# Kernel optimization log

Measured on AMD Instinct MI355X. Metric: run time of the kernel, lower is better.

Reference implementation:

```python
import jax, jax.numpy as jnp
import numpy as np
import math

D_MODEL = 1024
N_HEADS = 16
D_HEAD = D_MODEL // N_HEADS


def _pos_encoding(seq_len, d_model):
    # matches get_pos_encoding: paired frequencies (repeat_interleave(2)),
    # sin on even columns, cos on odd columns of the SAME angle matrix.
    position = jnp.arange(seq_len, dtype=jnp.float32)[:, None]          # [L,1]
    div = 1.0 / (10000.0 ** (jnp.arange(0, d_model, 2, dtype=jnp.float32) / d_model))
    div = jnp.repeat(div, 2)[None, :]                                    # [1,D]
    ang = position * div                                                 # [L,D]
    col = jnp.arange(d_model)
    return jnp.where(col[None, :] % 2 == 0, jnp.sin(ang), jnp.cos(ang))


def _rel_enc_shift(a):
    # a: [b, h, l, m] -> Transformer-XL relative shift
    b, h, l, m = a.shape
    a = jnp.concatenate([a, jnp.zeros((b, h, l, 1), a.dtype)], axis=-1)  # [b,h,l,m+1]
    a = a.reshape(b, h, l * (m + 1))
    a = a[:, :, l - 1: l - 1 + l * m]
    return a.reshape(b, h, l, m)


def setup_inputs() -> dict:
    key = jax.random.key(0)
    ks = jax.random.split(key, 10)
    B, S, D = 1, 2048, D_MODEL
    s = 1.0 / math.sqrt(D)
    inp = {
        "query": jax.random.normal(ks[0], (B, S, D), jnp.float32),
        "key": jax.random.normal(ks[1], (B, S, D), jnp.float32),
        "value": jax.random.normal(ks[2], (B, S, D), jnp.float32),
        "attn_mask": jnp.zeros((1, 1, S, S), jnp.float32),
        "Wq": jax.random.normal(ks[3], (D, D), jnp.float32) * s,
        "Wke": jax.random.normal(ks[4], (D, D), jnp.float32) * s,
        "Wkr": jax.random.normal(ks[5], (D, D), jnp.float32) * s,
        "Wv": jax.random.normal(ks[6], (D, D), jnp.float32) * s,
        "Wf": jax.random.normal(ks[7], (D, D), jnp.float32) * s,
        "u_param": jax.random.normal(ks[8], (1, 1, N_HEADS, D_HEAD), jnp.float32),
        "v_param": jax.random.normal(ks[9], (1, 1, N_HEADS, D_HEAD), jnp.float32),
    }
    return inp


def reference(query, key, value, attn_mask, Wq, Wke, Wkr, Wv, Wf, u_param, v_param):
    B, S, D = query.shape
    F = key.shape[1]
    H, dh = u_param.shape[2], u_param.shape[3]
    sqrt_dk = math.sqrt(D)

    rel_enc = _pos_encoding(F, D)[::-1, :]                     # flipped along seq dim

    q = (query @ Wq.T).reshape(B, S, H, dh)
    k = (key @ Wke.T).reshape(B, F, H, dh)
    v = (value @ Wv.T).reshape(B, F, H, dh)

    A_C = jnp.einsum('bsnd,bfnd->bnsf', q + u_param, k)
    Q = (rel_enc @ Wkr.T).reshape(F, H, dh)
    B_D_hat = jnp.einsum('bsnd,fnd->bnsf', q + v_param, Q)
    B_D = _rel_enc_shift(B_D_hat)

    score = (A_C + B_D) / sqrt_dk + attn_mask
    weights = jax.nn.softmax(score, axis=-1)                   # [B,H,S,F]
    attention_loss = jnp.mean(jnp.max(weights, axis=(-1, -2)))

    out = jnp.einsum('bnsf,bfnd->bsnd', weights, v).reshape(B, S, D)
    out = jax.nn.gelu(out @ Wf.T, approximate=False)
    return out, weights, attention_loss
```

## Files before the change

### kernel.cpp

```cpp
#include <hip/hip_runtime.h>
#include <math.h>

#define SEQ 2048
#define DMODEL 1024
#define NHEADS 16
#define DHEAD 64

#define LSLOTS 64
#define LSTRIDE 32

typedef long long i64;
typedef unsigned short u16;
typedef __attribute__((ext_vector_type(4))) float f32x4;
typedef __attribute__((ext_vector_type(8))) short bf16x8;

#define IN_E  2097152
#define W_E   1048576
#define HEAD_E 131072

__device__ inline u16 f2bf(float x) {
    union { float f; unsigned u; } v; v.f = x;
    unsigned r = v.u + 0x7FFF + ((v.u >> 16) & 1);
    return (u16)(r >> 16);
}
__device__ inline float bf2f(u16 h) {
    union { unsigned u; float f; } v; v.u = ((unsigned)h) << 16;
    return v.f;
}

__device__ inline void gload16(const void* g, void* l) {
    __builtin_amdgcn_global_load_lds(
        (const __attribute__((address_space(1))) unsigned int*)g,
        (__attribute__((address_space(3))) unsigned int*)l, 16, 0, 0);
}

struct SplitArgs {
    const float* src[8];
    u16* dh[8];
    u16* dl[8];
    int n4[8];
};
__global__ __launch_bounds__(256)
void split_all(SplitArgs a)
{
    const int z = blockIdx.y;
    const int i = blockIdx.x * 256 + threadIdx.x;
    if (i >= a.n4[z]) return;
    const float4 x = ((const float4*)a.src[z])[i];
    u16 h0 = f2bf(x.x), h1 = f2bf(x.y), h2 = f2bf(x.z), h3 = f2bf(x.w);
    u16 l0 = f2bf(x.x - bf2f(h0)), l1 = f2bf(x.y - bf2f(h1));
    u16 l2 = f2bf(x.z - bf2f(h2)), l3 = f2bf(x.w - bf2f(h3));
    uint2 hh; hh.x = (unsigned)h0 | ((unsigned)h1 << 16); hh.y = (unsigned)h2 | ((unsigned)h3 << 16);
    uint2 ll; ll.x = (unsigned)l0 | ((unsigned)l1 << 16); ll.y = (unsigned)l2 | ((unsigned)l3 << 16);
    ((uint2*)a.dh[z])[i] = hh;
    ((uint2*)a.dl[z])[i] = ll;
}

__global__ __launch_bounds__(256)
void posenc_split(u16* __restrict__ dh, u16* __restrict__ dl)
{
    const int idx = blockIdx.x * 256 + threadIdx.x;
    const int f = idx >> 10;
    const int i = idx & 1023;
    const float P = (float)(SEQ - 1 - f);
    const float ex = (float)(i & ~1) * (1.f / 1024.f);
    const float dv = powf(10000.f, -ex);
    const float ang = P * dv;
    const float val = (i & 1) ? cosf(ang) : sinf(ang);
    const u16 hb = f2bf(val);
    dh[idx] = hb;
    dl[idx] = f2bf(val - bf2f(hb));
}

struct TNArgs {
    const u16 *Ah, *Al, *Bh, *Bl;
    i64 sAz, sBz;
    float* Cf; i64 sCz; int ldc;
    u16 *O1h, *O1l, *O2h, *O2l;
    const float *b1, *b2;
    int K, mode;
};

__global__ __launch_bounds__(256)
void mfma_tn128(TNArgs p)
{
    __shared__ __align__(16) u16 Ash[128 * 32];
    __shared__ __align__(16) u16 Asl[128 * 32];
    __shared__ __align__(16) u16 Bsh[128 * 32];
    __shared__ __align__(16) u16 Bsl[128 * 32];
    const int tid = threadIdx.x, wave = tid >> 6, lane = tid & 63;
    const int z = blockIdx.z;
    const i64 m0 = (i64)blockIdx.y * 128, n0 = (i64)blockIdx.x * 128;
    const int K = p.K;
    const u16* Abh = p.Ah + (i64)z * p.sAz;
    const u16* Abl = p.Al + (i64)z * p.sAz;
    const u16* Bbh = p.Bh + (i64)z * p.sBz;
    const u16* Bbl = p.Bl + (i64)z * p.sBz;
    const int r0 = tid >> 2, kc = (tid & 3) * 8;
    const int r1 = r0 + 64;
    u16* dA0 = &Ash[wave * 512];
    u16* dA1 = &Ash[2048 + wave * 512];
    u16* dA0l = &Asl[wave * 512];
    u16* dA1l = &Asl[2048 + wave * 512];
    u16* dB0 = &Bsh[wave * 512];
    u16* dB1 = &Bsh[2048 + wave * 512];
    u16* dB0l = &Bsl[wave * 512];
    u16* dB1l = &Bsl[2048 + wave * 512];
    const int wm = (wave >> 1) * 64, wn = (wave & 1) * 64;
    f32x4 acc[4][4] = {};

    for (int k0 = 0; k0 < K; k0 += 32) {
        __syncthreads();
        const i64 ga0 = (m0 + r0) * K + k0 + kc;
        const i64 ga1 = (m0 + r1) * K + k0 + kc;
        const i64 gb0 = (n0 + r0) * K + k0 + kc;
        const i64 gb1 = (n0 + r1) * K + k0 + kc;
        gload16(Abh + ga0, dA0);  gload16(Abh + ga1, dA1);
        gload16(Abl + ga0, dA0l); gload16(Abl + ga1, dA1l);
        gload16(Bbh + gb0, dB0);  gload16(Bbh + gb1, dB1);
        gload16(Bbl + gb0, dB0l); gload16(Bbl + gb1, dB1l);
        __syncthreads();
        const int fr = lane & 15, fk = (lane >> 4) * 8;
        bf16x8 fah[4], fal[4], fbh[4], fbl[4];
#pragma unroll
        for (int t = 0; t < 4; ++t) {
            fah[t] = *(const bf16x8*)&Ash[(wm + t * 16 + fr) * 32 + fk];
            fal[t] = *(const bf16x8*)&Asl[(wm + t * 16 + fr) * 32 + fk];
            fbh[t] = *(const bf16x8*)&Bsh[(wn + t * 16 + fr) * 32 + fk];
            fbl[t] = *(const bf16x8*)&Bsl[(wn + t * 16 + fr) * 32 + fk];
        }
#pragma unroll
        for (int mi = 0; mi < 4; ++mi)
#pragma unroll
            for (int ni = 0; ni < 4; ++ni) {
                acc[mi][ni] = __builtin_amdgcn_mfma_f32_16x16x32_bf16(fah[mi], fbh[ni], acc[mi][ni], 0, 0, 0);
                acc[mi][ni] = __builtin_amdgcn_mfma_f32_16x16x32_bf16(fah[mi], fbl[ni], acc[mi][ni], 0, 0, 0);
                acc[mi][ni] = __builtin_amdgcn_mfma_f32_16x16x32_bf16(fal[mi], fbh[ni], acc[mi][ni], 0, 0, 0);
            }
    }

    const int fr = lane & 15, fq = (lane >> 4) * 4;
    if (p.mode == 0) {
        float* C = p.Cf + (i64)z * p.sCz;
#pragma unroll
        for (int mi = 0; mi < 4; ++mi)
#pragma unroll
            for (int e = 0; e < 4; ++e) {
                const i64 row = m0 + wm + mi * 16 + fq + e;
#pragma unroll
                for (int ni = 0; ni < 4; ++ni)
                    C[row * p.ldc + n0 + wn + ni * 16 + fr] = acc[mi][ni][e];
            }
    } else if (p.mode == 1) {
        const i64 obase = (i64)z * IN_E;
#pragma unroll
        for (int mi = 0; mi < 4; ++mi)
#pragma unroll
            for (int e = 0; e < 4; ++e) {
                const i64 m = m0 + wm + mi * 16 + fq + e;
#pragma unroll
                for (int ni = 0; ni < 4; ++ni) {
                    const int c = (int)n0 + wn + ni * 16 + fr;
                    const int h = c >> 6, d = c & 63;
                    const i64 off = ((i64)h * SEQ + m) * DHEAD + d;
                    float v = acc[mi][ni][e];
                    if (z == 0) v += p.b1[c];
                    const u16 hb = f2bf(v);
                    const u16 lb = f2bf(v - bf2f(hb));
                    p.O1h[obase + off] = hb;
                    p.O1l[obase + off] = lb;
                    if (z == 0) {
                        const float v2 = acc[mi][ni][e] + p.b2[c];
                        const u16 hb2 = f2bf(v2);
                        const u16 lb2 = f2bf(v2 - bf2f(hb2));
                        p.O2h[off] = hb2;
                        p.O2l[off] = lb2;
                    }
                }
            }
    } else {
        float* C = p.Cf;
#pragma unroll
        for (int mi = 0; mi < 4; ++mi)
#pragma unroll
            for (int e = 0; e < 4; ++e) {
                const i64 row = m0 + wm + mi * 16 + fq + e;
#pragma unroll
                for (int ni = 0; ni < 4; ++ni) {
                    const float x = acc[mi][ni][e];
                    C[row * p.ldc + n0 + wn + ni * 16 + fr] =
                        0.5f * x * (1.f + erff(x * 0.70710678118654752f));
                }
            }
    }
}

__global__ __launch_bounds__(256)
void mfma_pv(const float* __restrict__ Wgt, const u16* __restrict__ VTh,
             const u16* __restrict__ VTl, u16* __restrict__ Oh, u16* __restrict__ Ol)
{
    __shared__ __align__(16) float Asf[256 * 32];
    __shared__ __align__(16) u16 Bsh[64 * 32];
    __shared__ __align__(16) u16 Bsl[64 * 32];
    const int tid = threadIdx.x, wave = tid >> 6, lane = tid & 63;
    const int z = blockIdx.z;
    const i64 m0 = (i64)blockIdx.y * 256;
    const float* A = Wgt + (i64)z * SEQ * SEQ;
    const u16* Bh = VTh + (i64)z * HEAD_E;
    const u16* Bl = VTl + (i64)z * HEAD_E;
    const int ar = tid >> 3, akc = (tid & 7) * 4;
    const int br = tid >> 2, bkc = (tid & 3) * 8;
    const int wm = wave * 64;
    f32x4 acc[4][4] = {};

    for (int k0 = 0; k0 < SEQ; k0 += 32) {
        __syncthreads();
#pragma unroll
        for (int i = 0; i < 8; ++i)
            gload16(A + (m0 + ar + i * 32) * SEQ + k0 + akc, &Asf[(i * 256 + wave * 64) * 4]);
        gload16(Bh + (i64)br * SEQ + k0 + bkc, &Bsh[wave * 512]);
        gload16(Bl + (i64)br * SEQ + k0 + bkc, &Bsl[wave * 512]);
        __syncthreads();
        const int fr = lane & 15, fk = (lane >> 4) * 8;
        bf16x8 fbh[4], fbl[4];
#pragma unroll
        for (int t = 0; t < 4; ++t) {
            fbh[t] = *(const bf16x8*)&Bsh[(t * 16 + fr) * 32 + fk];
            fbl[t] = *(const bf16x8*)&Bsl[(t * 16 + fr) * 32 + fk];
        }
#pragma unroll
        for (int mi = 0; mi < 4; ++mi) {
            const float4 x0 = *(const float4*)&Asf[(wm + mi * 16 + fr) * 32 + fk];
            const float4 x1 = *(const float4*)&Asf[(wm + mi * 16 + fr) * 32 + fk + 4];
            float av[8] = { x0.x, x0.y, x0.z, x0.w, x1.x, x1.y, x1.z, x1.w };
            bf16x8 ah, al;
#pragma unroll
            for (int j = 0; j < 8; ++j) {
                union { float f; unsigned u; } v; v.f = av[j];
                const u16 hb = (u16)(v.u >> 16);
                union { unsigned u; float f; } fh; fh.u = v.u & 0xFFFF0000u;
                union { float f; unsigned u; } rm; rm.f = av[j] - fh.f;
                ah[j] = (short)hb;
                al[j] = (short)(u16)(rm.u >> 16);
            }
#pragma unroll
            for (int ni = 0; ni < 4; ++ni) {
                acc[mi][ni] = __builtin_amdgcn_mfma_f32_16x16x32_bf16(ah, fbh[ni], acc[mi][ni], 0, 0, 0);
                acc[mi][ni] = __builtin_amdgcn_mfma_f32_16x16x32_bf16(ah, fbl[ni], acc[mi][ni], 0, 0, 0);
                acc[mi][ni] = __builtin_amdgcn_mfma_f32_16x16x32_bf16(al, fbh[ni], acc[mi][ni], 0, 0, 0);
            }
        }
    }

    const int fr = lane & 15, fq = (lane >> 4) * 4;
#pragma unroll
    for (int mi = 0; mi < 4; ++mi)
#pragma unroll
        for (int e = 0; e < 4; ++e) {
            const i64 m = m0 + wm + mi * 16 + fq + e;
#pragma unroll
            for (int ni = 0; ni < 4; ++ni) {
                const int c = z * 64 + ni * 16 + fr;
                const float v = acc[mi][ni][e];
                const u16 hb = f2bf(v);
                Oh[m * DMODEL + c] = hb;
                Ol[m * DMODEL + c] = f2bf(v - bf2f(hb));
            }
        }
}

__global__ __launch_bounds__(256)
void transpose_vv(const u16* __restrict__ vh, const u16* __restrict__ vl,
                  u16* __restrict__ th, u16* __restrict__ tl)
{
    __shared__ u16 tile[64][65];
    const int tid = threadIdx.x;
    const int h = blockIdx.y, f0 = blockIdx.x * 64;
    const i64 src = ((i64)h * SEQ + f0) * DHEAD;
    const i64 dst = (i64)h * HEAD_E + f0;
#pragma unroll
    for (int i = 0; i < 16; ++i) {
        const int idx = i * 256 + tid;
        const int r = idx >> 6, c = idx & 63;
        tile[c][r] = vh[src + (i64)r * 64 + c];
    }
    __syncthreads();
#pragma unroll
    for (int i = 0; i < 16; ++i) {
        const int idx = i * 256 + tid;
        const int d = idx >> 6, fl = idx & 63;
        th[dst + (i64)d * SEQ + fl] = tile[d][fl];
    }
    __syncthreads();
#pragma unroll
    for (int i = 0; i < 16; ++i) {
        const int idx = i * 256 + tid;
        const int r = idx >> 6, c = idx & 63;
        tile[c][r] = vl[src + (i64)r * 64 + c];
    }
    __syncthreads();
#pragma unroll
    for (int i = 0; i < 16; ++i) {
        const int idx = i * 256 + tid;
        const int d = idx >> 6, fl = idx & 63;
        tl[dst + (i64)d * SEQ + fl] = tile[d][fl];
    }
}

__global__ __launch_bounds__(256)
void softmax_rows(float* __restrict__ Wbase, const float* __restrict__ Gbase,
                  const float* __restrict__ mask, unsigned int* __restrict__ lmin, int h0)
{
    __shared__ float red[4];
    const int hl = blockIdx.y;
    float* Wh = Wbase + (i64)(h0 + hl) * SEQ * SEQ;
    const float* G = Gbase + (i64)hl * SEQ * SEQ;
    const int i = blockIdx.x;
    const int tx = threadIdx.x;
    const i64 rowoff = (i64)i * SEQ;
    float s[8];
    float mloc = -3.0e38f;
#pragma unroll
    for (int r = 0; r < 8; ++r) {
        const int j = tx + (r << 8);
        float bd;
        if (j <= i)          bd = G[rowoff + (SEQ - 1 - i + j)];
        else if (j == i + 1) bd = 0.f;
        else                 bd = G[rowoff + SEQ + (j - i - 2)];
        const float v = (Wh[rowoff + j] + bd) * 0.03125f + mask[rowoff + j];
        s[r] = v;
        mloc = fmaxf(mloc, v);
    }
#pragma unroll
    for (int o = 32; o > 0; o >>= 1) mloc = fmaxf(mloc, __shfl_xor(mloc, o));
    if ((tx & 63) == 0) red[tx >> 6] = mloc;
    __syncthreads();
    const float m = fmaxf(fmaxf(red[0], red[1]), fmaxf(red[2], red[3]));
    __syncthreads();
    float lsum = 0.f;
#pragma unroll
    for (int r = 0; r < 8; ++r) { s[r] = __expf(s[r] - m); lsum += s[r]; }
#pragma unroll
    for (int o = 32; o > 0; o >>= 1) lsum += __shfl_xor(lsum, o);
    if ((tx & 63) == 0) red[tx >> 6] = lsum;
    __syncthreads();
    const float l = red[0] + red[1] + red[2] + red[3];
    const float inv = 1.f / l;
#pragma unroll
    for (int r = 0; r < 8; ++r) Wh[rowoff + tx + (r << 8)] = s[r] * inv;
    if (tx == 0)
        atomicMin(&lmin[(((h0 + hl) << 6) + (i & (LSLOTS - 1))) * LSTRIDE],
                  __float_as_uint(l));
}

__global__ __launch_bounds__(1024)
void init_kernel(unsigned int* __restrict__ lmin)
{
    lmin[threadIdx.x * LSTRIDE] = 0x7F7FFFFFu;
}

__global__ __launch_bounds__(1024)
void loss_kernel(const unsigned int* __restrict__ lmin, float* __restrict__ out)
{
    __shared__ float hs[16];
    const int w = threadIdx.x >> 6;
    const int lane = threadIdx.x & 63;
    float l = __uint_as_float(lmin[threadIdx.x * LSTRIDE]);
#pragma unroll
    for (int o = 32; o > 0; o >>= 1) l = fminf(l, __shfl_xor(l, o));
    if (lane == 0) hs[w] = 1.f / l;
    __syncthreads();
    if (threadIdx.x == 0) {
        float v = 0.f;
#pragma unroll
        for (int h = 0; h < 16; ++h) v += hs[h];
        *out = v * (1.f / NHEADS);
    }
}

extern "C" void kernel_launch(void* const* d_in, const int* in_sizes, int n_in,
                              void* d_out, int out_size, void* d_ws, size_t ws_size,
                              hipStream_t stream)
{
    const float* query = (const float*)d_in[0];
    const float* key   = (const float*)d_in[1];
    const float* value = (const float*)d_in[2];
    const float* mask  = (const float*)d_in[3];
    const float* Wq    = (const float*)d_in[4];
    const float* Wke   = (const float*)d_in[5];
    const float* Wkr   = (const float*)d_in[6];
    const float* Wv    = (const float*)d_in[7];
    const float* Wf    = (const float*)d_in[8];
    const float* u_p   = (const float*)d_in[9];
    const float* v_p   = (const float*)d_in[10];

    float* out_final = (float*)d_out;
    float* weights   = out_final + (i64)SEQ * DMODEL;
    float* loss      = weights + (i64)NHEADS * SEQ * SEQ;

    char* w = (char*)d_ws;
    u16* in_h = (u16*)w;               w += (i64)4 * IN_E * 2;
    u16* in_l = (u16*)w;               w += (i64)4 * IN_E * 2;
    u16* W_h  = (u16*)w;               w += (i64)5 * W_E * 2;
    u16* W_l  = (u16*)w;               w += (i64)5 * W_E * 2;
    u16* P_h  = (u16*)w;               w += (i64)4 * IN_E * 2;
    u16* P_l  = (u16*)w;               w += (i64)4 * IN_E * 2;
    u16* qv_h = (u16*)w;               w += (i64)IN_E * 2;
    u16* qv_l = (u16*)w;               w += (i64)IN_E * 2;
    u16* vvT_h = (u16*)w;              w += (i64)IN_E * 2;
    u16* vvT_l = (u16*)w;              w += (i64)IN_E * 2;
    u16* o_h  = (u16*)w;               w += (i64)IN_E * 2;
    u16* o_l  = (u16*)w;               w += (i64)IN_E * 2;
    unsigned int* lmin = (unsigned int*)w; w += (i64)NHEADS * LSLOTS * LSTRIDE * 4;
    const i64 fixed_bytes = (i64)(w - (char*)d_ws);
    const i64 gbytes = (i64)SEQ * SEQ * 4;
    const i64 avail = (i64)ws_size - fixed_bytes;
    float* G;
    int chunk;
    if (avail >= gbytes) {
        G = (float*)w;
        i64 ch = avail / gbytes;
        chunk = ch > 16 ? 16 : (int)ch;
    } else {
        G = (float*)in_h;
        chunk = 2;
    }

    dim3 blk(256);
    init_kernel<<<dim3(1), dim3(1024), 0, stream>>>(lmin);

    SplitArgs sa;
    sa.src[0] = query; sa.dh[0] = in_h;           sa.dl[0] = in_l;           sa.n4[0] = IN_E / 4;
    sa.src[1] = key;   sa.dh[1] = in_h + IN_E;    sa.dl[1] = in_l + IN_E;    sa.n4[1] = IN_E / 4;
    sa.src[2] = value; sa.dh[2] = in_h + 2*IN_E;  sa.dl[2] = in_l + 2*IN_E;  sa.n4[2] = IN_E / 4;
    sa.src[3] = Wq;    sa.dh[3] = W_h;            sa.dl[3] = W_l;            sa.n4[3] = W_E / 4;
    sa.src[4] = Wke;   sa.dh[4] = W_h + W_E;      sa.dl[4] = W_l + W_E;      sa.n4[4] = W_E / 4;
    sa.src[5] = Wv;    sa.dh[5] = W_h + 2*W_E;    sa.dl[5] = W_l + 2*W_E;    sa.n4[5] = W_E / 4;
    sa.src[6] = Wkr;   sa.dh[6] = W_h + 3*W_E;    sa.dl[6] = W_l + 3*W_E;    sa.n4[6] = W_E / 4;
    sa.src[7] = Wf;    sa.dh[7] = W_h + 4*W_E;    sa.dl[7] = W_l + 4*W_E;    sa.n4[7] = W_E / 4;
    split_all<<<dim3(2048, 8), blk, 0, stream>>>(sa);
    posenc_split<<<dim3(IN_E / 256), blk, 0, stream>>>(in_h + 3*(i64)IN_E, in_l + 3*(i64)IN_E);

    {
        TNArgs p = {};
        p.Ah = in_h; p.Al = in_l; p.Bh = W_h; p.Bl = W_l;
        p.sAz = IN_E; p.sBz = W_E;
        p.O1h = P_h; p.O1l = P_l; p.O2h = qv_h; p.O2l = qv_l;
        p.b1 = u_p; p.b2 = v_p;
        p.K = DMODEL; p.mode = 1;
        mfma_tn128<<<dim3(DMODEL / 128, SEQ / 128, 4), blk, 0, stream>>>(p);
    }

    transpose_vv<<<dim3(SEQ / 64, NHEADS), blk, 0, stream>>>(
        P_h + 2*(i64)IN_E, P_l + 2*(i64)IN_E, vvT_h, vvT_l);

    {
        TNArgs p = {};
        p.Ah = P_h; p.Al = P_l;
        p.Bh = P_h + IN_E; p.Bl = P_l + IN_E;
        p.sAz = HEAD_E; p.sBz = HEAD_E;
        p.Cf = weights; p.sCz = (i64)SEQ * SEQ; p.ldc = SEQ;
        p.K = DHEAD; p.mode = 0;
        mfma_tn128<<<dim3(SEQ / 128, SEQ / 128, NHEADS), blk, 0, stream>>>(p);
    }

    for (int h0 = 0; h0 < NHEADS; h0 += chunk) {
        const int ch = (h0 + chunk <= NHEADS) ? chunk : (NHEADS - h0);
        TNArgs p = {};
        p.Ah = qv_h + (i64)h0 * HEAD_E; p.Al = qv_l + (i64)h0 * HEAD_E;
        p.Bh = P_h + 3*(i64)IN_E + (i64)h0 * HEAD_E;
        p.Bl = P_l + 3*(i64)IN_E + (i64)h0 * HEAD_E;
        p.sAz = HEAD_E; p.sBz = HEAD_E;
        p.Cf = G; p.sCz = (i64)SEQ * SEQ; p.ldc = SEQ;
        p.K = DHEAD; p.mode = 0;
        mfma_tn128<<<dim3(SEQ / 128, SEQ / 128, ch), blk, 0, stream>>>(p);
        softmax_rows<<<dim3(SEQ, ch), blk, 0, stream>>>(weights, G, mask, lmin, h0);
    }

    mfma_pv<<<dim3(1, SEQ / 256, NHEADS), blk, 0, stream>>>(weights, vvT_h, vvT_l, o_h, o_l);

    {
        TNArgs p = {};
        p.Ah = o_h; p.Al = o_l;
        p.Bh = W_h + 4*(i64)W_E; p.Bl = W_l + 4*(i64)W_E;
        p.sAz = 0; p.sBz = 0;
        p.Cf = out_final; p.sCz = 0; p.ldc = DMODEL;
        p.K = DMODEL; p.mode = 2;
        mfma_tn128<<<dim3(DMODEL / 128, SEQ / 128, 1), blk, 0, stream>>>(p);
    }

    loss_kernel<<<dim3(1), dim3(1024), 0, stream>>>(lmin, loss);
}
```

Baseline: 626.7 us.

## Apply relative shift in BD GEMM epilogue and use one-wave-per-row vectorized softmax

The BD GEMM epilogue now writes each score directly to its relative-shifted position, so the softmax kernel reads G contiguously and no longer needs gathered, branchy index arithmetic. The softmax kernel is restructured so that each wave owns one row, uses float4 loads and stores, and reduces with shuffles only, removing the shared-memory reductions and block barriers. This trades coalesced GEMM stores for scattered, diagonal-shifted stores in the epilogue. The element at j==i+1 is never written and is instead special-cased to zero.

```diff
diff --git a/kernel.cpp b/kernel.cpp
--- a/kernel.cpp
+++ b/kernel.cpp
@@ -151,6 +151,22 @@
                 for (int ni = 0; ni < 4; ++ni)
                     C[row * p.ldc + n0 + wn + ni * 16 + fr] = acc[mi][ni][e];
             }
+    } else if (p.mode == 3) {
+        float* C = p.Cf + (i64)z * p.sCz;
+#pragma unroll
+        for (int mi = 0; mi < 4; ++mi)
+#pragma unroll
+            for (int e = 0; e < 4; ++e) {
+                const int r = (int)(m0 + wm + mi * 16 + fq + e);
+#pragma unroll
+                for (int ni = 0; ni < 4; ++ni) {
+                    const int f = (int)n0 + wn + ni * 16 + fr;
+                    if (f >= SEQ - 1 - r)
+                        C[(i64)r * SEQ + (f + r - (SEQ - 1))] = acc[mi][ni][e];
+                    else if (r >= 1)
+                        C[(i64)(r - 1) * SEQ + (f + r + 1)] = acc[mi][ni][e];
+                }
+            }
     } else if (p.mode == 1) {
         const i64 obase = (i64)z * IN_E;
 #pragma unroll
@@ -311,46 +327,52 @@
 void softmax_rows(float* __restrict__ Wbase, const float* __restrict__ Gbase,
                   const float* __restrict__ mask, unsigned int* __restrict__ lmin, int h0)
 {
-    __shared__ float red[4];
     const int hl = blockIdx.y;
     float* Wh = Wbase + (i64)(h0 + hl) * SEQ * SEQ;
-    const float* G = Gbase + (i64)hl * SEQ * SEQ;
-    const int i = blockIdx.x;
-    const int tx = threadIdx.x;
+    const float* Gs = Gbase + (i64)hl * SEQ * SEQ;
+    const int wave = threadIdx.x >> 6, lane = threadIdx.x & 63;
+    const int i = blockIdx.x * 4 + wave;
     const i64 rowoff = (i64)i * SEQ;
-    float s[8];
+    float s[32];
     float mloc = -3.0e38f;
 #pragma unroll
-    for (int r = 0; r < 8; ++r) {
-        const int j = tx + (r << 8);
-        float bd;
-        if (j <= i)          bd = G[rowoff + (SEQ - 1 - i + j)];
-        else if (j == i + 1) bd = 0.f;
-        else                 bd = G[rowoff + SEQ + (j - i - 2)];
-        const float v = (Wh[rowoff + j] + bd) * 0.03125f + mask[rowoff + j];
-        s[r] = v;
-        mloc = fmaxf(mloc, v);
+    for (int k = 0; k < 8; ++k) {
+        const int j = k * 256 + lane * 4;
+        const float4 wv = *(const float4*)&Wh[rowoff + j];
+        const float4 gv = *(const float4*)&Gs[rowoff + j];
+        const float4 mk = *(const float4*)&mask[rowoff + j];
+        const float wa[4] = { wv.x, wv.y, wv.z, wv.w };
+        const float ga[4] = { gv.x, gv.y, gv.z, gv.w };
+        const float ma[4] = { mk.x, mk.y, mk.z, mk.w };
+#pragma unroll
+        for (int e = 0; e < 4; ++e) {
+            const float bd = (j + e == i + 1) ? 0.f : ga[e];
+            const float v = (wa[e] + bd) * 0.03125f + ma[e];
+            s[k * 4 + e] = v;
+            mloc = fmaxf(mloc, v);
+        }
     }
 #pragma unroll
     for (int o = 32; o > 0; o >>= 1) mloc = fmaxf(mloc, __shfl_xor(mloc, o));
-    if ((tx & 63) == 0) red[tx >> 6] = mloc;
-    __syncthreads();
-    const float m = fmaxf(fmaxf(red[0], red[1]), fmaxf(red[2], red[3]));
-    __syncthreads();
     float lsum = 0.f;
 #pragma unroll
-    for (int r = 0; r < 8; ++r) { s[r] = __expf(s[r] - m); lsum += s[r]; }
+    for (int r = 0; r < 32; ++r) { s[r] = __expf(s[r] - mloc); lsum += s[r]; }
 #pragma unroll
     for (int o = 32; o > 0; o >>= 1) lsum += __shfl_xor(lsum, o);
-    if ((tx & 63) == 0) red[tx >> 6] = lsum;
-    __syncthreads();
-    const float l = red[0] + red[1] + red[2] + red[3];
-    const float inv = 1.f / l;
-#pragma unroll
-    for (int r = 0; r < 8; ++r) Wh[rowoff + tx + (r << 8)] = s[r] * inv;
-    if (tx == 0)
+    const float inv = 1.f / lsum;
+#pragma unroll
+    for (int k = 0; k < 8; ++k) {
+        const int j = k * 256 + lane * 4;
+        float4 ov;
+        ov.x = s[k * 4 + 0] * inv;
+        ov.y = s[k * 4 + 1] * inv;
+        ov.z = s[k * 4 + 2] * inv;
+        ov.w = s[k * 4 + 3] * inv;
+        *(float4*)&Wh[rowoff + j] = ov;
+    }
+    if (lane == 0)
         atomicMin(&lmin[(((h0 + hl) << 6) + (i & (LSLOTS - 1))) * LSTRIDE],
-                  __float_as_uint(l));
+                  __float_as_uint(lsum));
 }
 
 __global__ __launch_bounds__(1024)
@@ -472,9 +494,9 @@
         p.Bl = P_l + 3*(i64)IN_E + (i64)h0 * HEAD_E;
         p.sAz = HEAD_E; p.sBz = HEAD_E;
         p.Cf = G; p.sCz = (i64)SEQ * SEQ; p.ldc = SEQ;
-        p.K = DHEAD; p.mode = 0;
+        p.K = DHEAD; p.mode = 3;
         mfma_tn128<<<dim3(SEQ / 128, SEQ / 128, ch), blk, 0, stream>>>(p);
-        softmax_rows<<<dim3(SEQ, ch), blk, 0, stream>>>(weights, G, mask, lmin, h0);
+        softmax_rows<<<dim3(SEQ / 4, ch), blk, 0, stream>>>(weights, G, mask, lmin, h0);
     }
 
     mfma_pv<<<dim3(1, SEQ / 256, NHEADS), blk, 0, stream>>>(weights, vvT_h, vvT_l, o_h, o_l);
```

Measured after the change: 680.9 us. +8.7%, slower.

## Fuse score GEMMs, relative shift and softmax into one LDS-resident kernel

Applied to the files above, without the earlier changes.

Replaces the separate A_C GEMM (written into weights), the B_D GEMM into a global scratch buffer, and the row softmax with one kernel. Each block of 1024 threads computes 16 full score rows for a head in shared memory, applies the relative shift while storing the B_D tile, adds A_C, then does the softmax and writes the weights once. The aim is to remove two full SxS float writes and reads per head through global memory. In exchange, each block re-reads all K and R rows for only 16 query rows, and the large shared buffer limits occupancy to one block per CU.

```diff
diff --git a/kernel.cpp b/kernel.cpp
--- a/kernel.cpp
+++ b/kernel.cpp
@@ -140,18 +140,7 @@
     }
 
     const int fr = lane & 15, fq = (lane >> 4) * 4;
-    if (p.mode == 0) {
-        float* C = p.Cf + (i64)z * p.sCz;
-#pragma unroll
-        for (int mi = 0; mi < 4; ++mi)
-#pragma unroll
-            for (int e = 0; e < 4; ++e) {
-                const i64 row = m0 + wm + mi * 16 + fq + e;
-#pragma unroll
-                for (int ni = 0; ni < 4; ++ni)
-                    C[row * p.ldc + n0 + wn + ni * 16 + fr] = acc[mi][ni][e];
-            }
-    } else if (p.mode == 1) {
+    if (p.mode == 1) {
         const i64 obase = (i64)z * IN_E;
 #pragma unroll
         for (int mi = 0; mi < 4; ++mi)
@@ -195,6 +184,155 @@
     }
 }
 
+__global__ __launch_bounds__(1024, 1)
+void score_softmax(const u16* __restrict__ QUh, const u16* __restrict__ QUl,
+                   const u16* __restrict__ KKh, const u16* __restrict__ KKl,
+                   const u16* __restrict__ QVh, const u16* __restrict__ QVl,
+                   const u16* __restrict__ RRh, const u16* __restrict__ RRl,
+                   const float* __restrict__ mask, float* __restrict__ Wout,
+                   unsigned int* __restrict__ lmin)
+{
+    __shared__ __align__(16) float S[16][2052];
+    const int tid = threadIdx.x, wave = tid >> 6, lane = tid & 63;
+    const int h = blockIdx.y;
+    const int r0 = blockIdx.x * 16;
+    const i64 hb = (i64)h * HEAD_E;
+    const int n = lane & 15;
+    const int kc8 = (lane >> 4) * 8;
+
+    bf16x8 qa[2][2], va[2][2], vb[2][2];
+    {
+        const i64 mo = hb + (i64)(r0 + n) * 64 + kc8;
+#pragma unroll
+        for (int ks = 0; ks < 2; ++ks) {
+            qa[ks][0] = *(const bf16x8*)&QUh[mo + ks * 32];
+            qa[ks][1] = *(const bf16x8*)&QUl[mo + ks * 32];
+            va[ks][0] = *(const bf16x8*)&QVh[mo + ks * 32];
+            va[ks][1] = *(const bf16x8*)&QVl[mo + ks * 32];
+        }
+    }
+    const int fmaxB = 2031 - r0;
+    if (fmaxB > 0) {
+        const i64 mo = hb + (i64)(r0 + 16 + n) * 64 + kc8;
+#pragma unroll
+        for (int ks = 0; ks < 2; ++ks) {
+            vb[ks][0] = *(const bf16x8*)&QVh[mo + ks * 32];
+            vb[ks][1] = *(const bf16x8*)&QVl[mo + ks * 32];
+        }
+    }
+
+    if (tid < 16) S[tid][r0 + tid + 1] = 0.f;
+
+    for (int t = wave; t < 128; t += 16) {
+        const int ft = t * 16;
+        const i64 ao = hb + (i64)(ft + n) * 64 + kc8;
+        const bf16x8 a0h = *(const bf16x8*)&RRh[ao];
+        const bf16x8 a0l = *(const bf16x8*)&RRl[ao];
+        const bf16x8 a1h = *(const bf16x8*)&RRh[ao + 32];
+        const bf16x8 a1l = *(const bf16x8*)&RRl[ao + 32];
+        f32x4 a = {};
+        a = __builtin_amdgcn_mfma_f32_16x16x32_bf16(a0h, va[0][0], a, 0, 0, 0);
+        a = __builtin_amdgcn_mfma_f32_16x16x32_bf16(a0h, va[0][1], a, 0, 0, 0);
+        a = __builtin_amdgcn_mfma_f32_16x16x32_bf16(a0l, va[0][0], a, 0, 0, 0);
+        a = __builtin_amdgcn_mfma_f32_16x16x32_bf16(a1h, va[1][0], a, 0, 0, 0);
+        a = __builtin_amdgcn_mfma_f32_16x16x32_bf16(a1h, va[1][1], a, 0, 0, 0);
+        a = __builtin_amdgcn_mfma_f32_16x16x32_bf16(a1l, va[1][0], a, 0, 0, 0);
+        const int r = r0 + n;
+        const int fb = ft + (lane >> 4) * 4;
+#pragma unroll
+        for (int e = 0; e < 4; ++e) {
+            const int f = fb + e;
+            if (f >= 2047 - r)      S[n][f + r - 2047] = a[e];
+            else if (n >= 1)        S[n - 1][f + r + 1] = a[e];
+        }
+    }
+    for (int t = wave; t * 16 < fmaxB; t += 16) {
+        const int ft = t * 16;
+        const i64 ao = hb + (i64)(ft + n) * 64 + kc8;
+        const bf16x8 a0h = *(const bf16x8*)&RRh[ao];
+        const bf16x8 a0l = *(const bf16x8*)&RRl[ao];
+        const bf16x8 a1h = *(const bf16x8*)&RRh[ao + 32];
+        const bf16x8 a1l = *(const bf16x8*)&RRl[ao + 32];
+        f32x4 a = {};
+        a = __builtin_amdgcn_mfma_f32_16x16x32_bf16(a0h, vb[0][0], a, 0, 0, 0);
+        a = __builtin_amdgcn_mfma_f32_16x16x32_bf16(a0h, vb[0][1], a, 0, 0, 0);
+        a = __builtin_amdgcn_mfma_f32_16x16x32_bf16(a0l, vb[0][0], a, 0, 0, 0);
+        a = __builtin_amdgcn_mfma_f32_16x16x32_bf16(a1h, vb[1][0], a, 0, 0, 0);
+        a = __builtin_amdgcn_mfma_f32_16x16x32_bf16(a1h, vb[1][1], a, 0, 0, 0);
+        a = __builtin_amdgcn_mfma_f32_16x16x32_bf16(a1l, vb[1][0], a, 0, 0, 0);
+        if (n == 0) {
+            const int fb = ft + (lane >> 4) * 4;
+#pragma unroll
+            for (int e = 0; e < 4; ++e) {
+                const int f = fb + e;
+                if (f < fmaxB) S[15][f + r0 + 17] = a[e];
+            }
+        }
+    }
+    __syncthreads();
+
+    for (int t = wave; t < 128; t += 16) {
+        const int ft = t * 16;
+        const i64 ao = hb + (i64)(ft + n) * 64 + kc8;
+        const bf16x8 a0h = *(const bf16x8*)&KKh[ao];
+        const bf16x8 a0l = *(const bf16x8*)&KKl[ao];
+        const bf16x8 a1h = *(const bf16x8*)&KKh[ao + 32];
+        const bf16x8 a1l = *(const bf16x8*)&KKl[ao + 32];
+        f32x4 a = {};
+        a = __builtin_amdgcn_mfma_f32_16x16x32_bf16(a0h, qa[0][0], a, 0, 0, 0);
+        a = __builtin_amdgcn_mfma_f32_16x16x32_bf16(a0h, qa[0][1], a, 0, 0, 0);
+        a = __builtin_amdgcn_mfma_f32_16x16x32_bf16(a0l, qa[0][0], a, 0, 0, 0);
+        a = __builtin_amdgcn_mfma_f32_16x16x32_bf16(a1h, qa[1][0], a, 0, 0, 0);
+        a = __builtin_amdgcn_mfma_f32_16x16x32_bf16(a1h, qa[1][1], a, 0, 0, 0);
+        a = __builtin_amdgcn_mfma_f32_16x16x32_bf16(a1l, qa[1][0], a, 0, 0, 0);
+        const int fb = ft + (lane >> 4) * 4;
+        f32x4* p = (f32x4*)&S[n][fb];
+        *p = *p + a;
+    }
+    __syncthreads();
+
+    const int lr = wave;
+    const int irow = r0 + lr;
+    const float* mrow = mask + (i64)irow * SEQ;
+    float sv[32];
+    float mloc = -3.0e38f;
+#pragma unroll
+    for (int q = 0; q < 8; ++q) {
+        const int j = q * 256 + lane * 4;
+        const f32x4 x = *(const f32x4*)&S[lr][j];
+        const float4 mk = *(const float4*)&mrow[j];
+        const float m4[4] = { mk.x, mk.y, mk.z, mk.w };
+#pragma unroll
+        for (int e = 0; e < 4; ++e) {
+            const float v = x[e] * 0.03125f + m4[e];
+            sv[q * 4 + e] = v;
+            mloc = fmaxf(mloc, v);
+        }
+    }
+#pragma unroll
+    for (int o = 32; o > 0; o >>= 1) mloc = fmaxf(mloc, __shfl_xor(mloc, o));
+    float lsum = 0.f;
+#pragma unroll
+    for (int q = 0; q < 32; ++q) { sv[q] = __expf(sv[q] - mloc); lsum += sv[q]; }
+#pragma unroll
+    for (int o = 32; o > 0; o >>= 1) lsum += __shfl_xor(lsum, o);
+    const float inv = 1.f / lsum;
+    float* wrow = Wout + (i64)h * SEQ * SEQ + (i64)irow * SEQ;
+#pragma unroll
+    for (int q = 0; q < 8; ++q) {
+        const int j = q * 256 + lane * 4;
+        float4 ov;
+        ov.x = sv[q * 4 + 0] * inv;
+        ov.y = sv[q * 4 + 1] * inv;
+        ov.z = sv[q * 4 + 2] * inv;
+        ov.w = sv[q * 4 + 3] * inv;
+        *(float4*)&wrow[j] = ov;
+    }
+    if (lane == 0)
+        atomicMin(&lmin[(((unsigned)h << 6) + (irow & (LSLOTS - 1))) * LSTRIDE],
+                  __float_as_uint(lsum));
+}
+
 __global__ __launch_bounds__(256)
 void mfma_pv(const float* __restrict__ Wgt, const u16* __restrict__ VTh,
              const u16* __restrict__ VTl, u16* __restrict__ Oh, u16* __restrict__ Ol)
@@ -305,52 +443,6 @@
         const int d = idx >> 6, fl = idx & 63;
         tl[dst + (i64)d * SEQ + fl] = tile[d][fl];
     }
-}
-
-__global__ __launch_bounds__(256)
-void softmax_rows(float* __restrict__ Wbase, const float* __restrict__ Gbase,
-                  const float* __restrict__ mask, unsigned int* __restrict__ lmin, int h0)
-{
-    __shared__ float red[4];
-    const int hl = blockIdx.y;
-    float* Wh = Wbase + (i64)(h0 + hl) * SEQ * SEQ;
-    const float* G = Gbase + (i64)hl * SEQ * SEQ;
-    const int i = blockIdx.x;
-    const int tx = threadIdx.x;
-    const i64 rowoff = (i64)i * SEQ;
-    float s[8];
-    float mloc = -3.0e38f;
-#pragma unroll
-    for (int r = 0; r < 8; ++r) {
-        const int j = tx + (r << 8);
-        float bd;
-        if (j <= i)          bd = G[rowoff + (SEQ - 1 - i + j)];
-        else if (j == i + 1) bd = 0.f;
-        else                 bd = G[rowoff + SEQ + (j - i - 2)];
-        const float v = (Wh[rowoff + j] + bd) * 0.03125f + mask[rowoff + j];
-        s[r] = v;
-        mloc = fmaxf(mloc, v);
-    }
-#pragma unroll
-    for (int o = 32; o > 0; o >>= 1) mloc = fmaxf(mloc, __shfl_xor(mloc, o));
-    if ((tx & 63) == 0) red[tx >> 6] = mloc;
-    __syncthreads();
-    const float m = fmaxf(fmaxf(red[0], red[1]), fmaxf(red[2], red[3]));
-    __syncthreads();
-    float lsum = 0.f;
-#pragma unroll
-    for (int r = 0; r < 8; ++r) { s[r] = __expf(s[r] - m); lsum += s[r]; }
-#pragma unroll
-    for (int o = 32; o > 0; o >>= 1) lsum += __shfl_xor(lsum, o);
-    if ((tx & 63) == 0) red[tx >> 6] = lsum;
-    __syncthreads();
-    const float l = red[0] + red[1] + red[2] + red[3];
-    const float inv = 1.f / l;
-#pragma unroll
-    for (int r = 0; r < 8; ++r) Wh[rowoff + tx + (r << 8)] = s[r] * inv;
-    if (tx == 0)
-        atomicMin(&lmin[(((h0 + hl) << 6) + (i & (LSLOTS - 1))) * LSTRIDE],
-                  __float_as_uint(l));
 }
 
 __global__ __launch_bounds__(1024)
@@ -412,19 +504,6 @@
     u16* o_h  = (u16*)w;               w += (i64)IN_E * 2;
     u16* o_l  = (u16*)w;               w += (i64)IN_E * 2;
     unsigned int* lmin = (unsigned int*)w; w += (i64)NHEADS * LSLOTS * LSTRIDE * 4;
-    const i64 fixed_bytes = (i64)(w - (char*)d_ws);
-    const i64 gbytes = (i64)SEQ * SEQ * 4;
-    const i64 avail = (i64)ws_size - fixed_bytes;
-    float* G;
-    int chunk;
-    if (avail >= gbytes) {
-        G = (float*)w;
-        i64 ch = avail / gbytes;
-        chunk = ch > 16 ? 16 : (int)ch;
-    } else {
-        G = (float*)in_h;
-        chunk = 2;
-    }
 
     dim3 blk(256);
     init_kernel<<<dim3(1), dim3(1024), 0, stream>>>(lmin);
@@ -454,28 +533,12 @@
     transpose_vv<<<dim3(SEQ / 64, NHEADS), blk, 0, stream>>>(
         P_h + 2*(i64)IN_E, P_l + 2*(i64)IN_E, vvT_h, vvT_l);
 
-    {
-        TNArgs p = {};
-        p.Ah = P_h; p.Al = P_l;
-        p.Bh = P_h + IN_E; p.Bl = P_l + IN_E;
-        p.sAz = HEAD_E; p.sBz = HEAD_E;
-        p.Cf = weights; p.sCz = (i64)SEQ * SEQ; p.ldc = SEQ;
-        p.K = DHEAD; p.mode = 0;
-        mfma_tn128<<<dim3(SEQ / 128, SEQ / 128, NHEADS), blk, 0, stream>>>(p);
-    }
-
-    for (int h0 = 0; h0 < NHEADS; h0 += chunk) {
-        const int ch = (h0 + chunk <= NHEADS) ? chunk : (NHEADS - h0);
-        TNArgs p = {};
-        p.Ah = qv_h + (i64)h0 * HEAD_E; p.Al = qv_l + (i64)h0 * HEAD_E;
-        p.Bh = P_h + 3*(i64)IN_E + (i64)h0 * HEAD_E;
-        p.Bl = P_l + 3*(i64)IN_E + (i64)h0 * HEAD_E;
-        p.sAz = HEAD_E; p.sBz = HEAD_E;
-        p.Cf = G; p.sCz = (i64)SEQ * SEQ; p.ldc = SEQ;
-        p.K = DHEAD; p.mode = 0;
-        mfma_tn128<<<dim3(SEQ / 128, SEQ / 128, ch), blk, 0, stream>>>(p);
-        softmax_rows<<<dim3(SEQ, ch), blk, 0, stream>>>(weights, G, mask, lmin, h0);
-    }
+    score_softmax<<<dim3(SEQ / 16, NHEADS), dim3(1024), 0, stream>>>(
+        P_h, P_l,
+        P_h + IN_E, P_l + IN_E,
+        qv_h, qv_l,
+        P_h + 3*(i64)IN_E, P_l + 3*(i64)IN_E,
+        mask, weights, lmin);
 
     mfma_pv<<<dim3(1, SEQ / 256, NHEADS), blk, 0, stream>>>(weights, vvT_h, vvT_l, o_h, o_l);
 
```

New measurement: 681.2 us. 8.7% more time.
